# Kernel tuning notes

Hardware: AMD Instinct MI355X
Metric: run time of the kernel (lower is better)

## Reference

```python
import jax, jax.numpy as jnp
import numpy as np

N_NODES = 100000
N_EDGES = 1600000
IN_DIM = 128
HID = 64
HEADS = 1
NEG_SLOPE = 0.2


def setup_inputs() -> dict:
    key = jax.random.key(0)
    ks = jax.random.split(key, 12)
    def xavier(k, shape):
        fan_in, fan_out = shape[-2], shape[-1]
        lim = jnp.sqrt(6.0 / (fan_in + fan_out))
        return jax.random.uniform(k, shape, jnp.float32, -lim, lim)
    x = jax.random.normal(ks[0], (N_NODES, IN_DIM), jnp.float32)
    edge_index = jax.random.randint(ks[1], (2, N_EDGES), 0, N_NODES, jnp.int64)
    # layer 0: in 128 -> heads*hid (64)
    W0 = xavier(ks[2], (IN_DIM, HEADS * HID))
    al0 = xavier(ks[3], (1, HEADS, HID))
    ar0 = xavier(ks[4], (1, HEADS, HID))
    # layer 1: in heads*hid (64) -> 64
    W1 = xavier(ks[5], (HEADS * HID, HEADS * HID))
    al1 = xavier(ks[6], (1, HEADS, HID))
    ar1 = xavier(ks[7], (1, HEADS, HID))
    # post_mp: Linear(64,64) -> Linear(64,64)
    Wp1 = xavier(ks[8], (HEADS * HID, HID))
    bp1 = jnp.zeros((HID,), jnp.float32)
    Wp2 = xavier(ks[9], (HID, HID))
    bp2 = jnp.zeros((HID,), jnp.float32)
    return {"x": x, "edge_index": edge_index, "W0": W0, "al0": al0, "ar0": ar0,
            "W1": W1, "al1": al1, "ar1": ar1, "Wp1": Wp1, "bp1": bp1,
            "Wp2": Wp2, "bp2": bp2}


def gat_layer(x, W, att_l, att_r, src, dst, n_nodes):
    H, C = att_l.shape[1], att_l.shape[2]
    # lin_l == lin_r (shared weight), no bias
    xh = (x @ W).reshape(n_nodes, H, C)            # [N,H,C]
    alpha_l = jnp.sum(xh * att_l, axis=-1)         # [N,H]
    alpha_r = jnp.sum(xh * att_r, axis=-1)         # [N,H]
    # per-edge logit: alpha_i (dst) + alpha_j (src)
    a = alpha_l[src] + alpha_r[dst]                # [E,H]
    a = jnp.where(a >= 0, a, NEG_SLOPE * a)        # leaky_relu
    # segment softmax over incoming edges of each dst node
    amax = jax.ops.segment_max(a, dst, num_segments=n_nodes)
    e = jnp.exp(a - amax[dst])
    denom = jax.ops.segment_sum(e, dst, num_segments=n_nodes)
    alpha = e / (denom[dst] + 1e-16)               # [E,H]
    msg = xh[src] * alpha[:, :, None]              # [E,H,C]
    out = jax.ops.segment_sum(msg, dst, num_segments=n_nodes)  # [N,H,C]
    return out.reshape(n_nodes, H * C)


def reference(x, edge_index, W0, al0, ar0, W1, al1, ar1, Wp1, bp1, Wp2, bp2):
    src, dst = edge_index[0], edge_index[1]
    n = x.shape[0]
    h = gat_layer(x, W0, al0, ar0, src, dst, n)
    h = jax.nn.relu(h)
    h = gat_layer(h, W1, al1, ar1, src, dst, n)
    h = jax.nn.relu(h)
    # post_mp (dropout inactive in eval)
    h = h @ Wp1 + bp1
    h = h @ Wp2 + bp2
    return h  # emb=True -> return embedding
```

## Files before the change

### kernel.cpp

```cpp
#include <hip/hip_runtime.h>
#include <math.h>

#define NEG_SLOPE 0.2f
#define CAP 8192

typedef _Float16 half8 __attribute__((ext_vector_type(8)));
typedef _Float16 half4v __attribute__((ext_vector_type(4)));
typedef float float4v __attribute__((ext_vector_type(4)));

__global__ void setup_misc(const float* __restrict__ W0, const float* __restrict__ W1,
                           const float* __restrict__ Wp1, const float* __restrict__ Wp2,
                           _Float16* __restrict__ W0T, _Float16* __restrict__ W1T,
                           _Float16* __restrict__ Wp1T, _Float16* __restrict__ Wp2T,
                           int* __restrict__ cursor, int NB) {
    const int tid = threadIdx.x;
    if (blockIdx.x == 4) {
        for (int t = tid; t < NB; t += 256) cursor[t] = t * CAP;
        return;
    }
    __shared__ float lds[128 * 64];
    const float* src; _Float16* dstp; int K;
    switch (blockIdx.x) {
        case 0: src = W0;  dstp = W0T;  K = 128; break;
        case 1: src = W1;  dstp = W1T;  K = 64;  break;
        case 2: src = Wp1; dstp = Wp1T; K = 64;  break;
        default: src = Wp2; dstp = Wp2T; K = 64; break;
    }
    for (int i = tid; i < K * 64; i += 256) lds[i] = src[i];
    __syncthreads();
    for (int i = tid; i < K * 64; i += 256) {
        int n = i / K, k = i % K;
        dstp[i] = (_Float16)lds[k * 64 + n];
    }
}

__global__ void bin_staged(const int* __restrict__ src, const int* __restrict__ dst,
                           int* __restrict__ cursor, unsigned int* __restrict__ packed,
                           int E, int NB) {
    __shared__ unsigned int sval[4096];
    __shared__ unsigned int saddr[4096];
    __shared__ int h[512], hcur[512], gb[512];
    __shared__ int stot;
    const int tid = threadIdx.x;
    if (tid == 0) stot = 0;
    for (int t = tid; t < NB; t += 256) h[t] = 0;
    __syncthreads();
    const int base = blockIdx.x * 4096;
    const int lim = min(base + 4096, E);
    int dreg[16], sreg[16];
    int cnt = 0;
    for (int i = base + tid; i < lim; i += 256) {
        dreg[cnt] = dst[i];
        sreg[cnt] = src[i];
        ++cnt;
    }
    for (int k = 0; k < cnt; ++k) atomicAdd(&h[dreg[k] >> 8], 1);
    __syncthreads();
    for (int t = tid; t < NB; t += 256) {
        int c = h[t];
        if (c) {
            int l = atomicAdd(&stot, c);
            hcur[t] = l;
            gb[t] = atomicAdd(&cursor[t], c) - l;
        }
    }
    __syncthreads();
    for (int k = 0; k < cnt; ++k) {
        const int d = dreg[k];
        const int b = d >> 8;
        const int pos = atomicAdd(&hcur[b], 1);
        sval[pos] = ((unsigned int)(d & 255) << 24) | (unsigned int)sreg[k];
        saddr[pos] = (unsigned int)(gb[b] + pos);
    }
    __syncthreads();
    const int tot = stot;
    for (int j = tid; j < tot; j += 256)
        packed[saddr[j]] = sval[j];
}

__device__ __forceinline__ void sort_body(const unsigned int* __restrict__ packed,
                                          const int* __restrict__ cursor,
                                          int* __restrict__ csr, int2* __restrict__ rr,
                                          int N, int b) {
    __shared__ int hist[256], cur[256];
    __shared__ int wsum[4], woff[4];
    const int tid = threadIdx.x, wid = tid >> 6, lane = tid & 63;
    const int beg = b * CAP;
    const int end = cursor[b];
    hist[tid] = 0;
    __syncthreads();
    for (int i = beg + tid; i < end; i += 256)
        atomicAdd(&hist[packed[i] >> 24], 1);
    __syncthreads();
    int v = hist[tid];
    int x = v;
    #pragma unroll
    for (int off = 1; off < 64; off <<= 1) {
        int t = __shfl_up(x, off);
        if (lane >= off) x += t;
    }
    if (lane == 63) wsum[wid] = x;
    __syncthreads();
    if (tid == 0) {
        int acc = 0;
        #pragma unroll
        for (int w = 0; w < 4; ++w) { woff[w] = acc; acc += wsum[w]; }
    }
    __syncthreads();
    int excl = woff[wid] + x - v;
    int node = (b << 8) + tid;
    if (node < N) rr[node] = make_int2(beg + excl, v);
    cur[tid] = excl;
    __syncthreads();
    for (int i = beg + tid; i < end; i += 256) {
        unsigned int p = packed[i];
        int pos = atomicAdd(&cur[p >> 24], 1);
        csr[beg + pos] = (int)(p & 0xFFFFFFu);
    }
}

__device__ __forceinline__ void gemm0_body(const float* __restrict__ X,
                                           const _Float16* __restrict__ WT,
                                           const float* __restrict__ alw,
                                           const float* __restrict__ arw,
                                           _Float16* __restrict__ XH,
                                           float* __restrict__ AL, float* __restrict__ AR,
                                           int N, int bid) {
    const int wid = threadIdx.x >> 6, lane = threadIdx.x & 63;
    const int rowbase = bid * 64 + wid * 16;
    const int idx16 = lane & 15;
    const int g = lane >> 4;
    const int mrow = rowbase + idx16;
    const bool mvalid = (mrow < N);

    float4v acc[4];
    #pragma unroll
    for (int n = 0; n < 4; ++n) acc[n] = float4v{0.f, 0.f, 0.f, 0.f};

    #pragma unroll
    for (int ks = 0; ks < 4; ++ks) {
        const int k0 = ks * 32 + g * 8;
        half8 a = {};
        if (mvalid) {
            const float* xp = X + (size_t)mrow * 128 + k0;
            float4v lo = *reinterpret_cast<const float4v*>(xp);
            float4v hi = *reinterpret_cast<const float4v*>(xp + 4);
            #pragma unroll
            for (int i = 0; i < 4; ++i) {
                a[i] = (_Float16)lo[i];
                a[i + 4] = (_Float16)hi[i];
            }
        }
        #pragma unroll
        for (int n = 0; n < 4; ++n) {
            const half8 b = *reinterpret_cast<const half8*>(WT + (size_t)(n * 16 + idx16) * 128 + k0);
            acc[n] = __builtin_amdgcn_mfma_f32_16x16x32_f16(a, b, acc[n], 0, 0, 0);
        }
    }

    float alv[4], arv[4];
    #pragma unroll
    for (int n = 0; n < 4; ++n) { alv[n] = alw[n * 16 + idx16]; arv[n] = arw[n * 16 + idx16]; }
    #pragma unroll
    for (int r = 0; r < 4; ++r) {
        const int row = rowbase + g * 4 + r;
        if (row < N) {
            float pl = 0.f, pr = 0.f;
            #pragma unroll
            for (int n = 0; n < 4; ++n) {
                float vv = acc[n][r];
                XH[(size_t)row * 64 + n * 16 + idx16] = (_Float16)vv;
                pl = fmaf(vv, alv[n], pl);
                pr = fmaf(vv, arv[n], pr);
            }
            pl += __shfl_xor(pl, 1); pr += __shfl_xor(pr, 1);
            pl += __shfl_xor(pl, 2); pr += __shfl_xor(pr, 2);
            pl += __shfl_xor(pl, 4); pr += __shfl_xor(pr, 4);
            pl += __shfl_xor(pl, 8); pr += __shfl_xor(pr, 8);
            if (idx16 == 0) { AL[row] = pl; AR[row] = pr; }
        }
    }
}

__global__ void sort_and_gemm0(const unsigned int* __restrict__ packed,
                               const int* __restrict__ cursor,
                               int* __restrict__ csr, int2* __restrict__ rr,
                               const float* __restrict__ X,
                               const _Float16* __restrict__ W0T,
                               const float* __restrict__ alw, const float* __restrict__ arw,
                               _Float16* __restrict__ XH0, float* __restrict__ AL0,
                               float* __restrict__ AR0, int N, int NB) {
    if ((int)blockIdx.x < NB)
        sort_body(packed, cursor, csr, rr, N, blockIdx.x);
    else
        gemm0_body(X, W0T, alw, arw, XH0, AL0, AR0, N, blockIdx.x - NB);
}


__device__ __forceinline__ void agg_phase(const int2* __restrict__ rr,
                                          const int* __restrict__ csr,
                                          const float* __restrict__ ALp,
                                          const float* __restrict__ ARp,
                                          const _Float16* __restrict__ XHp,
                                          _Float16* ts, int nb, int N) {
    const int tid = threadIdx.x;
    const int l = tid & 15, grp = tid >> 4;
    const int node = nb + grp;
    float4v acc = {0.f, 0.f, 0.f, 0.f};
    float inv = 0.0f;
    if (node < N) {
        const int2 r = rr[node];
        const int beg = r.x, end = r.x + r.y;
        const float ar = ARp[node];
        float s = 0.f;
        for (int cbeg = beg; cbeg < end; cbeg += 16) {
            const int e = cbeg + l;
            const bool valid = (e < end);
            const int sidx = valid ? csr[e] : 0;
            float a = ALp[sidx] + ar;
            a = (a >= 0.0f) ? a : NEG_SLOPE * a;
            const float ex = valid ? __expf(a) : 0.0f;
            s += ex;
            #pragma unroll
            for (int j = 0; j < 16; ++j) {
                const float wgt = __shfl(ex, j, 16);
                const int si = __shfl(sidx, j, 16);
                const half4v h = *reinterpret_cast<const half4v*>(XHp + (size_t)si * 64 + l * 4);
                acc[0] = fmaf((float)h[0], wgt, acc[0]);
                acc[1] = fmaf((float)h[1], wgt, acc[1]);
                acc[2] = fmaf((float)h[2], wgt, acc[2]);
                acc[3] = fmaf((float)h[3], wgt, acc[3]);
            }
        }
        s += __shfl_xor(s, 1); s += __shfl_xor(s, 2);
        s += __shfl_xor(s, 4); s += __shfl_xor(s, 8);
        inv = 1.0f / (s + 1e-16f);
    }
    half4v o;
    o[0] = (_Float16)fmaxf(acc[0] * inv, 0.f);
    o[1] = (_Float16)fmaxf(acc[1] * inv, 0.f);
    o[2] = (_Float16)fmaxf(acc[2] * inv, 0.f);
    o[3] = (_Float16)fmaxf(acc[3] * inv, 0.f);
    const int hoff = (grp * 128 + ((l * 8) ^ ((grp & 7) << 4))) >> 1;
    *reinterpret_cast<half4v*>(ts + hoff) = o;
    __syncthreads();
}

__device__ __forceinline__ half8 ts_afrag(const _Float16* ts, int row, int kb) {
    return *reinterpret_cast<const half8*>(ts + ((row * 128 + (kb ^ ((row & 7) << 4))) >> 1));
}

__global__ void agg_gemm_mid(const int2* __restrict__ rr, const int* __restrict__ csr,
                             const float* __restrict__ AL0, const float* __restrict__ AR0,
                             const _Float16* __restrict__ XH0,
                             const _Float16* __restrict__ W1T,
                             const float* __restrict__ al1w, const float* __restrict__ ar1w,
                             _Float16* __restrict__ XH1, float* __restrict__ AL1,
                             float* __restrict__ AR1, int N) {
    __shared__ _Float16 ts[16 * 64];
    const int nb = blockIdx.x * 16;
    agg_phase(rr, csr, AL0, AR0, XH0, ts, nb, N);
    if (threadIdx.x >= 64) return;

    const int lane = threadIdx.x;
    const int idx16 = lane & 15, g = lane >> 4;
    float alv[4], arv[4];
    #pragma unroll
    for (int n = 0; n < 4; ++n) { alv[n] = al1w[n * 16 + idx16]; arv[n] = ar1w[n * 16 + idx16]; }

    float4v acc[4];
    #pragma unroll
    for (int n = 0; n < 4; ++n) acc[n] = float4v{0.f, 0.f, 0.f, 0.f};
    #pragma unroll
    for (int ks = 0; ks < 2; ++ks) {
        const half8 a = ts_afrag(ts, idx16, ks * 64 + g * 16);
        const int k0 = ks * 32 + g * 8;
        #pragma unroll
        for (int n = 0; n < 4; ++n) {
            const half8 b = *reinterpret_cast<const half8*>(W1T + (size_t)(n * 16 + idx16) * 64 + k0);
            acc[n] = __builtin_amdgcn_mfma_f32_16x16x32_f16(a, b, acc[n], 0, 0, 0);
        }
    }
    #pragma unroll
    for (int r = 0; r < 4; ++r) {
        const int row = nb + g * 4 + r;
        if (row < N) {
            float pl = 0.f, pr = 0.f;
            #pragma unroll
            for (int n = 0; n < 4; ++n) {
                float vv = acc[n][r];
                XH1[(size_t)row * 64 + n * 16 + idx16] = (_Float16)vv;
                pl = fmaf(vv, alv[n], pl);
                pr = fmaf(vv, arv[n], pr);
            }
            pl += __shfl_xor(pl, 1); pr += __shfl_xor(pr, 1);
            pl += __shfl_xor(pl, 2); pr += __shfl_xor(pr, 2);
            pl += __shfl_xor(pl, 4); pr += __shfl_xor(pr, 4);
            pl += __shfl_xor(pl, 8); pr += __shfl_xor(pr, 8);
            if (idx16 == 0) { AL1[row] = pl; AR1[row] = pr; }
        }
    }
}

__global__ void agg_post(const int2* __restrict__ rr, const int* __restrict__ csr,
                         const float* __restrict__ AL1, const float* __restrict__ AR1,
                         const _Float16* __restrict__ XH1,
                         const _Float16* __restrict__ Wp1T, const float* __restrict__ bp1,
                         const _Float16* __restrict__ Wp2T, const float* __restrict__ bp2,
                         float* __restrict__ OUT, int N) {
    __shared__ _Float16 ts[16 * 64];
    __shared__ _Float16 tls[16][72];
    const int nb = blockIdx.x * 16;
    agg_phase(rr, csr, AL1, AR1, XH1, ts, nb, N);
    if (threadIdx.x >= 64) return;

    const int lane = threadIdx.x;
    const int idx16 = lane & 15, g = lane >> 4;

    float4v acc1[4];
    #pragma unroll
    for (int n = 0; n < 4; ++n) acc1[n] = float4v{0.f, 0.f, 0.f, 0.f};
    #pragma unroll
    for (int ks = 0; ks < 2; ++ks) {
        const half8 a = ts_afrag(ts, idx16, ks * 64 + g * 16);
        const int k0 = ks * 32 + g * 8;
        #pragma unroll
        for (int n = 0; n < 4; ++n) {
            const half8 b = *reinterpret_cast<const half8*>(Wp1T + (size_t)(n * 16 + idx16) * 64 + k0);
            acc1[n] = __builtin_amdgcn_mfma_f32_16x16x32_f16(a, b, acc1[n], 0, 0, 0);
        }
    }
    #pragma unroll
    for (int r = 0; r < 4; ++r)
        #pragma unroll
        for (int n = 0; n < 4; ++n)
            tls[g * 4 + r][n * 16 + idx16] = (_Float16)(acc1[n][r] + bp1[n * 16 + idx16]);

    float4v acc2[4];
    #pragma unroll
    for (int n = 0; n < 4; ++n) acc2[n] = float4v{0.f, 0.f, 0.f, 0.f};
    #pragma unroll
    for (int ks = 0; ks < 2; ++ks) {
        const int k0 = ks * 32 + g * 8;
        const half8 a = *reinterpret_cast<const half8*>(&tls[idx16][k0]);
        #pragma unroll
        for (int n = 0; n < 4; ++n) {
            const half8 b = *reinterpret_cast<const half8*>(Wp2T + (size_t)(n * 16 + idx16) * 64 + k0);
            acc2[n] = __builtin_amdgcn_mfma_f32_16x16x32_f16(a, b, acc2[n], 0, 0, 0);
        }
    }
    #pragma unroll
    for (int r = 0; r < 4; ++r) {
        const int row = nb + g * 4 + r;
        if (row < N) {
            #pragma unroll
            for (int n = 0; n < 4; ++n)
                OUT[(size_t)row * 64 + n * 16 + idx16] = acc2[n][r] + bp2[n * 16 + idx16];
        }
    }
}

extern "C" void kernel_launch(void* const* d_in, const int* in_sizes, int n_in,
                              void* d_out, int out_size, void* d_ws, size_t ws_size,
                              hipStream_t stream) {
    const float* x   = (const float*)d_in[0];
    const int*   ei  = (const int*)d_in[1];
    const float* W0  = (const float*)d_in[2];
    const float* al0 = (const float*)d_in[3];
    const float* ar0 = (const float*)d_in[4];
    const float* W1  = (const float*)d_in[5];
    const float* al1 = (const float*)d_in[6];
    const float* ar1 = (const float*)d_in[7];
    const float* Wp1 = (const float*)d_in[8];
    const float* bp1 = (const float*)d_in[9];
    const float* Wp2 = (const float*)d_in[10];
    const float* bp2 = (const float*)d_in[11];
    float* out = (float*)d_out;

    const int N = in_sizes[0] / 128;
    const int E = in_sizes[1] / 2;
    const int* src = ei;
    const int* dst = ei + E;
    const int NB = (N + 255) >> 8;

    char* w = (char*)d_ws;
    _Float16* XH0  = (_Float16*)w;     w += sizeof(_Float16) * (size_t)N * 64;
    _Float16* XH1  = (_Float16*)w;     w += sizeof(_Float16) * (size_t)N * 64;
    float*  AL0    = (float*)w;        w += sizeof(float) * N;
    float*  AR0    = (float*)w;        w += sizeof(float) * N;
    float*  AL1    = (float*)w;        w += sizeof(float) * N;
    float*  AR1    = (float*)w;        w += sizeof(float) * N;
    int2*   rr     = (int2*)w;         w += sizeof(int2) * N;
    int*    csr    = (int*)w;          w += sizeof(int) * (size_t)NB * CAP;
    unsigned int* packed = (unsigned int*)w; w += sizeof(unsigned int) * (size_t)NB * CAP;
    int*    cursor = (int*)w;          w += sizeof(int) * 512;
    _Float16* W0T  = (_Float16*)w;     w += sizeof(_Float16) * 128 * 64;
    _Float16* W1T  = (_Float16*)w;     w += sizeof(_Float16) * 64 * 64;
    _Float16* Wp1T = (_Float16*)w;     w += sizeof(_Float16) * 64 * 64;
    _Float16* Wp2T = (_Float16*)w;

    dim3 blk(256);
    const int gn64 = (N + 63) / 64;
    const int gn16 = (N + 15) / 16;
    const int geb  = (E + 4095) / 4096;

    setup_misc<<<5, blk, 0, stream>>>(W0, W1, Wp1, Wp2, W0T, W1T, Wp1T, Wp2T,
                                      cursor, NB);

    bin_staged<<<geb, blk, 0, stream>>>(src, dst, cursor, packed, E, NB);

    sort_and_gemm0<<<NB + gn64, blk, 0, stream>>>(packed, cursor, csr, rr,
                                                  x, W0T, al0, ar0, XH0, AL0, AR0,
                                                  N, NB);

    agg_gemm_mid<<<gn16, blk, 0, stream>>>(rr, csr, AL0, AR0, XH0,
                                           W1T, al1, ar1, XH1, AL1, AR1, N);

    agg_post<<<gn16, blk, 0, stream>>>(rr, csr, AL1, AR1, XH1,
                                       Wp1T, bp1, Wp2T, bp2, out, N);
}
```

Before: 151.9 us.

## Use 8 lanes per node in aggregation with 16-byte gathers, 32 nodes per block

The aggregation phase now assigns 8 lanes per destination node instead of 16, so each lane gathers 8 halves (16 bytes) per neighbor row. Edges are processed in chunks of 8, and each 256-thread block covers 32 nodes. The follow-on MFMA GEMMs use two wavefronts, each on its own 16-row slice. The aim is wider, more efficient gathers and more nodes in flight per block with half the blocks. The cost is more accumulator registers per lane, and low-degree nodes waste lanes in a different pattern.

```diff
diff --git a/kernel.cpp b/kernel.cpp
--- a/kernel.cpp
+++ b/kernel.cpp
@@ -204,16 +204,16 @@
                                           const _Float16* __restrict__ XHp,
                                           _Float16* ts, int nb, int N) {
     const int tid = threadIdx.x;
-    const int l = tid & 15, grp = tid >> 4;
+    const int l = tid & 7, grp = tid >> 3;
     const int node = nb + grp;
-    float4v acc = {0.f, 0.f, 0.f, 0.f};
+    float accv[8] = {0.f, 0.f, 0.f, 0.f, 0.f, 0.f, 0.f, 0.f};
     float inv = 0.0f;
     if (node < N) {
         const int2 r = rr[node];
         const int beg = r.x, end = r.x + r.y;
         const float ar = ARp[node];
         float s = 0.f;
-        for (int cbeg = beg; cbeg < end; cbeg += 16) {
+        for (int cbeg = beg; cbeg < end; cbeg += 8) {
             const int e = cbeg + l;
             const bool valid = (e < end);
             const int sidx = valid ? csr[e] : 0;
@@ -222,27 +222,24 @@
             const float ex = valid ? __expf(a) : 0.0f;
             s += ex;
             #pragma unroll
-            for (int j = 0; j < 16; ++j) {
-                const float wgt = __shfl(ex, j, 16);
-                const int si = __shfl(sidx, j, 16);
-                const half4v h = *reinterpret_cast<const half4v*>(XHp + (size_t)si * 64 + l * 4);
-                acc[0] = fmaf((float)h[0], wgt, acc[0]);
-                acc[1] = fmaf((float)h[1], wgt, acc[1]);
-                acc[2] = fmaf((float)h[2], wgt, acc[2]);
-                acc[3] = fmaf((float)h[3], wgt, acc[3]);
+            for (int j = 0; j < 8; ++j) {
+                const float wgt = __shfl(ex, j, 8);
+                const int si = __shfl(sidx, j, 8);
+                const half8 h = *reinterpret_cast<const half8*>(XHp + (size_t)si * 64 + l * 8);
+                #pragma unroll
+                for (int i = 0; i < 8; ++i)
+                    accv[i] = fmaf((float)h[i], wgt, accv[i]);
             }
         }
-        s += __shfl_xor(s, 1); s += __shfl_xor(s, 2);
-        s += __shfl_xor(s, 4); s += __shfl_xor(s, 8);
+        s += __shfl_xor(s, 1); s += __shfl_xor(s, 2); s += __shfl_xor(s, 4);
         inv = 1.0f / (s + 1e-16f);
     }
-    half4v o;
-    o[0] = (_Float16)fmaxf(acc[0] * inv, 0.f);
-    o[1] = (_Float16)fmaxf(acc[1] * inv, 0.f);
-    o[2] = (_Float16)fmaxf(acc[2] * inv, 0.f);
-    o[3] = (_Float16)fmaxf(acc[3] * inv, 0.f);
-    const int hoff = (grp * 128 + ((l * 8) ^ ((grp & 7) << 4))) >> 1;
-    *reinterpret_cast<half4v*>(ts + hoff) = o;
+    half8 o;
+    #pragma unroll
+    for (int i = 0; i < 8; ++i)
+        o[i] = (_Float16)fmaxf(accv[i] * inv, 0.f);
+    const int hoff = (grp * 128 + ((l * 16) ^ ((grp & 7) << 4))) >> 1;
+    *reinterpret_cast<half8*>(ts + hoff) = o;
     __syncthreads();
 }
 
@@ -257,13 +254,14 @@
                              const float* __restrict__ al1w, const float* __restrict__ ar1w,
                              _Float16* __restrict__ XH1, float* __restrict__ AL1,
                              float* __restrict__ AR1, int N) {
-    __shared__ _Float16 ts[16 * 64];
-    const int nb = blockIdx.x * 16;
+    __shared__ _Float16 ts[32 * 64];
+    const int nb = blockIdx.x * 32;
     agg_phase(rr, csr, AL0, AR0, XH0, ts, nb, N);
-    if (threadIdx.x >= 64) return;
-
-    const int lane = threadIdx.x;
+    if (threadIdx.x >= 128) return;
+
+    const int wv = threadIdx.x >> 6, lane = threadIdx.x & 63;
     const int idx16 = lane & 15, g = lane >> 4;
+    const int rl = wv * 16;
     float alv[4], arv[4];
     #pragma unroll
     for (int n = 0; n < 4; ++n) { alv[n] = al1w[n * 16 + idx16]; arv[n] = ar1w[n * 16 + idx16]; }
@@ -273,7 +271,7 @@
     for (int n = 0; n < 4; ++n) acc[n] = float4v{0.f, 0.f, 0.f, 0.f};
     #pragma unroll
     for (int ks = 0; ks < 2; ++ks) {
-        const half8 a = ts_afrag(ts, idx16, ks * 64 + g * 16);
+        const half8 a = ts_afrag(ts, rl + idx16, ks * 64 + g * 16);
         const int k0 = ks * 32 + g * 8;
         #pragma unroll
         for (int n = 0; n < 4; ++n) {
@@ -283,7 +281,7 @@
     }
     #pragma unroll
     for (int r = 0; r < 4; ++r) {
-        const int row = nb + g * 4 + r;
+        const int row = nb + rl + g * 4 + r;
         if (row < N) {
             float pl = 0.f, pr = 0.f;
             #pragma unroll
@@ -308,21 +306,22 @@
                          const _Float16* __restrict__ Wp1T, const float* __restrict__ bp1,
                          const _Float16* __restrict__ Wp2T, const float* __restrict__ bp2,
                          float* __restrict__ OUT, int N) {
-    __shared__ _Float16 ts[16 * 64];
-    __shared__ _Float16 tls[16][72];
-    const int nb = blockIdx.x * 16;
+    __shared__ _Float16 ts[32 * 64];
+    __shared__ _Float16 tls[2][16][72];
+    const int nb = blockIdx.x * 32;
     agg_phase(rr, csr, AL1, AR1, XH1, ts, nb, N);
-    if (threadIdx.x >= 64) return;
-
-    const int lane = threadIdx.x;
+    if (threadIdx.x >= 128) return;
+
+    const int wv = threadIdx.x >> 6, lane = threadIdx.x & 63;
     const int idx16 = lane & 15, g = lane >> 4;
+    const int rl = wv * 16;
 
     float4v acc1[4];
     #pragma unroll
     for (int n = 0; n < 4; ++n) acc1[n] = float4v{0.f, 0.f, 0.f, 0.f};
     #pragma unroll
     for (int ks = 0; ks < 2; ++ks) {
-        const half8 a = ts_afrag(ts, idx16, ks * 64 + g * 16);
+        const half8 a = ts_afrag(ts, rl + idx16, ks * 64 + g * 16);
         const int k0 = ks * 32 + g * 8;
         #pragma unroll
         for (int n = 0; n < 4; ++n) {
@@ -334,7 +333,7 @@
     for (int r = 0; r < 4; ++r)
         #pragma unroll
         for (int n = 0; n < 4; ++n)
-            tls[g * 4 + r][n * 16 + idx16] = (_Float16)(acc1[n][r] + bp1[n * 16 + idx16]);
+            tls[wv][g * 4 + r][n * 16 + idx16] = (_Float16)(acc1[n][r] + bp1[n * 16 + idx16]);
 
     float4v acc2[4];
     #pragma unroll
@@ -342,7 +341,7 @@
     #pragma unroll
     for (int ks = 0; ks < 2; ++ks) {
         const int k0 = ks * 32 + g * 8;
-        const half8 a = *reinterpret_cast<const half8*>(&tls[idx16][k0]);
+        const half8 a = *reinterpret_cast<const half8*>(&tls[wv][idx16][k0]);
         #pragma unroll
         for (int n = 0; n < 4; ++n) {
             const half8 b = *reinterpret_cast<const half8*>(Wp2T + (size_t)(n * 16 + idx16) * 64 + k0);
@@ -351,7 +350,7 @@
     }
     #pragma unroll
     for (int r = 0; r < 4; ++r) {
-        const int row = nb + g * 4 + r;
+        const int row = nb + rl + g * 4 + r;
         if (row < N) {
             #pragma unroll
             for (int n = 0; n < 4; ++n)
@@ -401,7 +400,7 @@
 
     dim3 blk(256);
     const int gn64 = (N + 63) / 64;
-    const int gn16 = (N + 15) / 16;
+    const int gn32 = (N + 31) / 32;
     const int geb  = (E + 4095) / 4096;
 
     setup_misc<<<5, blk, 0, stream>>>(W0, W1, Wp1, Wp2, W0T, W1T, Wp1T, Wp2T,
@@ -413,9 +412,9 @@
                                                   x, W0T, al0, ar0, XH0, AL0, AR0,
                                                   N, NB);
 
-    agg_gemm_mid<<<gn16, blk, 0, stream>>>(rr, csr, AL0, AR0, XH0,
+    agg_gemm_mid<<<gn32, blk, 0, stream>>>(rr, csr, AL0, AR0, XH0,
                                            W1T, al1, ar1, XH1, AL1, AR1, N);
 
-    agg_post<<<gn16, blk, 0, stream>>>(rr, csr, AL1, AR1, XH1,
+    agg_post<<<gn32, blk, 0, stream>>>(rr, csr, AL1, AR1, XH1,
                                        Wp1T, bp1, Wp2T, bp2, out, N);
 }
```

After: 148.6 us. 1.02x faster.
